# Optimization experiments

Hardware: AMD Instinct MI355X
Metric: run time of the kernel (lower is better)

## Reference

```python
import jax, jax.numpy as jnp
import numpy as np


def setup_inputs() -> dict:
    key = jax.random.key(0)
    kx, kw, kb = jax.random.split(key, 3)
    x = jax.random.normal(kx, (4, 2048, 4096), dtype=jnp.float32)
    weight = jax.random.normal(kw, (4096, 4096), dtype=jnp.float32) * 0.02
    bias = jax.random.normal(kb, (4096,), dtype=jnp.float32) * 0.02
    return {"x": x, "weight": weight, "bias": bias}


def _binarize_except_outliers(w):
    # Outlier mask from global weight stats (computed from w itself; in torch it
    # is cached after the first call but the values are identical every step).
    mean = jnp.mean(w)
    std = jnp.std(w, ddof=1)  # torch.std default is the unbiased estimator
    lower = mean - 1.96 * std
    upper = mean + 1.96 * std
    outliers = (w < lower) | (w > upper)
    keep = (~outliers).astype(w.dtype)
    # scaling_factor in the torch code: w[~outliers].abs().mean(-1) on the
    # flattened masked-select -> a single SCALAR, detached from the graph.
    scale = jax.lax.stop_gradient(jnp.sum(jnp.abs(w) * keep) / jnp.sum(keep))
    # NOTE: the torch code assigns STE-sign values and then immediately
    # overwrites them with w * scale, so the effective math is:
    w_bin = jnp.where(outliers, w, w * scale)
    return w_bin


def reference(x, weight, bias):
    w_bin = _binarize_except_outliers(weight)  # [out, in]
    # F.linear(x, w, b) = x @ w.T + b
    return jnp.einsum("bsi,oi->bso", x, w_bin) + bias
```

## Files before the change

### kernel.cpp

```cpp
#include <hip/hip_runtime.h>
#include <hip/hip_bf16.h>
#include <math.h>

#define MDIM 8192
#define NDIM 4096
#define KDIM 4096
#define WELEMS 16777216
#define XELEMS 33554432

typedef __attribute__((ext_vector_type(8))) short bf16x8;
typedef __attribute__((ext_vector_type(4))) float f32x4;

__device__ __forceinline__ unsigned short f2bf(float f) {
  unsigned int u = __float_as_uint(f);
  u += 0x7fffu + ((u >> 16) & 1u);
  return (unsigned short)(u >> 16);
}

__device__ __forceinline__ void gload16(const void* g, void* l) {
  __builtin_amdgcn_global_load_lds(
      (const __attribute__((address_space(1))) void*)g,
      (__attribute__((address_space(3))) void*)l, 16, 0, 0);
}

template <int MODE>
__global__ __launch_bounds__(256)
void np_stage1(const float* __restrict__ w, float* __restrict__ C,
               float* __restrict__ C2, const float* __restrict__ scal) {
  __shared__ float ls[32], ls2[32];
  const int t = threadIdx.x;
  const int leaf = t >> 3, j = t & 7;
  const size_t base = (size_t)blockIdx.x * 4096 + leaf * 128 + j;
  float mean = 0.f, lower = 0.f, upper = 0.f;
  if (MODE == 1) mean = scal[0];
  if (MODE == 2) { lower = scal[1]; upper = scal[2]; }
  float r = 0.f, r2 = 0.f;
#pragma unroll
  for (int s = 0; s < 16; s++) {
    float v = w[base + s * 8];
    float tv, tv2 = 0.f;
    if (MODE == 0) tv = v;
    else if (MODE == 1) { float x = v - mean; tv = __fmul_rn(x, x); }
    else {
      bool keep = !(v < lower || v > upper);
      tv = keep ? fabsf(v) : 0.f;
      tv2 = keep ? 1.f : 0.f;
    }
    if (s == 0) { r = tv; r2 = tv2; } else { r += tv; r2 += tv2; }
  }
  r += __shfl_xor(r, 1); r += __shfl_xor(r, 2); r += __shfl_xor(r, 4);
  if (MODE == 2) { r2 += __shfl_xor(r2, 1); r2 += __shfl_xor(r2, 2); r2 += __shfl_xor(r2, 4); }
  if (j == 0) { ls[leaf] = r; if (MODE == 2) ls2[leaf] = r2; }
  __syncthreads();
  if (t == 0) {
    float tmp[32];
    for (int i = 0; i < 32; i++) tmp[i] = ls[i];
    for (int n = 32; n > 1; n >>= 1)
      for (int i = 0; i < n / 2; i++) tmp[i] = tmp[2 * i] + tmp[2 * i + 1];
    C[blockIdx.x] = tmp[0];
    if (MODE == 2) {
      for (int i = 0; i < 32; i++) tmp[i] = ls2[i];
      for (int n = 32; n > 1; n >>= 1)
        for (int i = 0; i < n / 2; i++) tmp[i] = tmp[2 * i] + tmp[2 * i + 1];
      C2[blockIdx.x] = tmp[0];
    }
  }
}

template <int MODE>
__global__ __launch_bounds__(256)
void np_stage2(const float* __restrict__ C, const float* __restrict__ C2,
               float* __restrict__ scal) {
  __shared__ float ls[256], ls2[256];
  const int t = threadIdx.x;
  {
    float v[16];
    for (int i = 0; i < 16; i++) v[i] = C[t * 16 + i];
    for (int n = 16; n > 1; n >>= 1)
      for (int i = 0; i < n / 2; i++) v[i] = v[2 * i] + v[2 * i + 1];
    ls[t] = v[0];
    if (MODE == 2) {
      for (int i = 0; i < 16; i++) v[i] = C2[t * 16 + i];
      for (int n = 16; n > 1; n >>= 1)
        for (int i = 0; i < n / 2; i++) v[i] = v[2 * i] + v[2 * i + 1];
      ls2[t] = v[0];
    }
  }
  __syncthreads();
  if (t == 0) {
    float tmp[256];
    for (int i = 0; i < 256; i++) tmp[i] = ls[i];
    for (int n = 256; n > 1; n >>= 1)
      for (int i = 0; i < n / 2; i++) tmp[i] = tmp[2 * i] + tmp[2 * i + 1];
    float S = tmp[0];
    if (MODE == 0) {
      scal[0] = S / 16777216.0f;
    } else if (MODE == 1) {
      float var = S / 16777215.0f;
      float sd = sqrtf(var);
      float mean = scal[0];
      scal[1] = mean - __fmul_rn(1.96f, sd);
      scal[2] = mean + __fmul_rn(1.96f, sd);
    } else {
      for (int i = 0; i < 256; i++) tmp[i] = ls2[i];
      for (int n = 256; n > 1; n >>= 1)
        for (int i = 0; i < n / 2; i++) tmp[i] = tmp[2 * i] + tmp[2 * i + 1];
      scal[3] = S / tmp[0];
    }
  }
}

__device__ __forceinline__ void pack8(const float* __restrict__ p, unsigned short* dst,
                                      bool dobin, float lower, float upper, float scale) {
  float4 u = *(const float4*)p;
  float4 v = *(const float4*)(p + 4);
  float f[8] = {u.x, u.y, u.z, u.w, v.x, v.y, v.z, v.w};
  unsigned int r[4];
#pragma unroll
  for (int j = 0; j < 4; j++) {
    float a = f[2 * j], b = f[2 * j + 1];
    if (dobin) {
      bool oa = (a < lower) || (a > upper);
      bool ob = (b < lower) || (b > upper);
      a = oa ? a : __fmul_rn(a, scale);
      b = ob ? b : __fmul_rn(b, scale);
    }
    r[j] = (unsigned int)f2bf(a) | ((unsigned int)f2bf(b) << 16);
  }
  *(uint4*)dst = make_uint4(r[0], r[1], r[2], r[3]);
}

__global__ __launch_bounds__(256)
void convert_w(const float* __restrict__ w, unsigned short* __restrict__ wb,
               const float* __restrict__ scal) {
  float lower = scal[1], upper = scal[2], scale = scal[3];
  int tid = blockIdx.x * blockDim.x + threadIdx.x;
  int nth = gridDim.x * blockDim.x;
  int nc = WELEMS / 8;
  for (int i = tid; i < nc; i += nth)
    pack8(w + (size_t)i * 8, wb + (size_t)i * 8, true, lower, upper, scale);
}

__global__ __launch_bounds__(256)
void convert_x(const float* __restrict__ x, unsigned short* __restrict__ xb) {
  int tid = blockIdx.x * blockDim.x + threadIdx.x;
  int nth = gridDim.x * blockDim.x;
  int nc = XELEMS / 8;
  for (int i = tid; i < nc; i += nth)
    pack8(x + (size_t)i * 8, xb + (size_t)i * 8, false, 0.f, 0.f, 0.f);
}


#define VM6  asm volatile("s_waitcnt vmcnt(6)" ::: "memory")
#define VM0  asm volatile("s_waitcnt vmcnt(0)" ::: "memory")
#define LGK8 asm volatile("s_waitcnt lgkmcnt(8)" ::: "memory")
#define PSYNC { asm volatile("" ::: "memory"); __builtin_amdgcn_s_barrier(); asm volatile("" ::: "memory"); }

#define LDA(buf, mh) { \
  a[0][0] = *(const bf16x8*)&sA[buf][wm][((mh)*64 +  0 + fr)*64 + koo0]; \
  a[0][1] = *(const bf16x8*)&sA[buf][wm][((mh)*64 +  0 + fr)*64 + koo1]; \
  a[1][0] = *(const bf16x8*)&sA[buf][wm][((mh)*64 + 16 + fr)*64 + koo0]; \
  a[1][1] = *(const bf16x8*)&sA[buf][wm][((mh)*64 + 16 + fr)*64 + koo1]; \
  a[2][0] = *(const bf16x8*)&sA[buf][wm][((mh)*64 + 32 + fr)*64 + koo0]; \
  a[2][1] = *(const bf16x8*)&sA[buf][wm][((mh)*64 + 32 + fr)*64 + koo1]; \
  a[3][0] = *(const bf16x8*)&sA[buf][wm][((mh)*64 + 48 + fr)*64 + koo0]; \
  a[3][1] = *(const bf16x8*)&sA[buf][wm][((mh)*64 + 48 + fr)*64 + koo1]; }

#define LDBX(buf, nh, bb) { \
  bb[0][0] = *(const bf16x8*)&sB[buf][wnh][(wnq*64 + (nh)*32 +  0 + fr)*64 + koo0]; \
  bb[0][1] = *(const bf16x8*)&sB[buf][wnh][(wnq*64 + (nh)*32 +  0 + fr)*64 + koo1]; \
  bb[1][0] = *(const bf16x8*)&sB[buf][wnh][(wnq*64 + (nh)*32 + 16 + fr)*64 + koo0]; \
  bb[1][1] = *(const bf16x8*)&sB[buf][wnh][(wnq*64 + (nh)*32 + 16 + fr)*64 + koo1]; }

#define MM1(m, n, ks, bb) acc[m][n] = __builtin_amdgcn_mfma_f32_16x16x32_bf16(a[(m)&3][ks], bb[(n)&1][ks], acc[m][n], 0, 0, 0)
#define MMKS(mh, nh, ks, bb) { \
  MM1((mh)*4+0, (nh)*2+0, ks, bb); MM1((mh)*4+0, (nh)*2+1, ks, bb); \
  MM1((mh)*4+1, (nh)*2+0, ks, bb); MM1((mh)*4+1, (nh)*2+1, ks, bb); \
  MM1((mh)*4+2, (nh)*2+0, ks, bb); MM1((mh)*4+2, (nh)*2+1, ks, bb); \
  MM1((mh)*4+3, (nh)*2+0, ks, bb); MM1((mh)*4+3, (nh)*2+1, ks, bb); }
#define MM(mh, nh, bb) { \
  __builtin_amdgcn_s_setprio(1); \
  MMKS(mh, nh, 0, bb); MMKS(mh, nh, 1, bb); \
  __builtin_amdgcn_s_setprio(0); }

#define STGA(buf, q, ku) { \
  gload16(xbp + aoff[0][q] + (ku), &sA[buf][0][(q)*4096 + t8]); \
  gload16(xbp + aoff[1][q] + (ku), &sA[buf][1][(q)*4096 + t8]); }
#define STGB(buf, h, ku) { \
  gload16(wbp + boff[h][0] + (ku), &sB[buf][h][t8]); \
  gload16(wbp + boff[h][1] + (ku), &sB[buf][h][4096 + t8]); }

__global__ __launch_bounds__(512, 2)
void gemm256(const unsigned short* __restrict__ xbp, const unsigned short* __restrict__ wbp,
             const float* __restrict__ bias, float* __restrict__ out) {
  __shared__ unsigned short sA[2][2][8192];
  __shared__ unsigned short sB[2][2][8192];

  const int bid = blockIdx.x;
  const int swz = (bid & 7) * 64 + (bid >> 3);
  const int bm = swz >> 4;
  const int bn = swz & 15;

  const int t = threadIdx.x;
  const int lane = t & 63;
  const int wid = t >> 6;
  const int wm = wid >> 2;
  const int wn = wid & 3;
  const int wnh = wn >> 1;
  const int wnq = wn & 1;
  const int fr = lane & 15;
  const int ko = (lane >> 4) * 8;
  const int xr = (fr & 7) << 3;
  const int koo0 = ko ^ xr;
  const int koo1 = (32 + ko) ^ xr;

  const int t8 = t * 8;
  const int rl = t >> 3;
  const int cs = ((t & 7) * 8) ^ ((rl & 7) << 3);
  size_t aoff[2][2], boff[2][2];
#pragma unroll
  for (int h = 0; h < 2; h++)
#pragma unroll
    for (int q = 0; q < 2; q++) {
      aoff[h][q] = (size_t)(bm * 256 + h * 128 + q * 64 + rl) * KDIM + cs;
      boff[h][q] = (size_t)(bn * 256 + h * 128 + q * 64 + rl) * KDIM + cs;
    }

  f32x4 acc[8][4];
#pragma unroll
  for (int i = 0; i < 8; i++)
#pragma unroll
    for (int j = 0; j < 4; j++) acc[i][j] = {0.f, 0.f, 0.f, 0.f};

  bf16x8 a[4][2], b0[2][2], b1[2][2];

  STGB(0, 0, 0); STGB(0, 1, 0); STGA(0, 0, 0); STGA(0, 1, 0);
  STGB(1, 0, 64); STGB(1, 1, 64); STGA(1, 0, 64);
  VM6; PSYNC;

  const int NIT = KDIM / 128;
  for (int it = 0; it < NIT; ++it) {
    const bool last = (it == NIT - 1);
    const int kuB = it * 128 + 64;
    const int kuN = kuB + 64;
    const int kuL = kuB + 128;

    LDA(0, 0); LDBX(0, 0, b0);
    STGA(1, 1, kuB);
    LGK8; PSYNC;
    MM(0, 0, b0); PSYNC;

    LDBX(0, 1, b1);
    PSYNC;
    MM(0, 1, b1); PSYNC;

    LDA(0, 1);
    if (!last) { STGB(0, 0, kuN); STGB(0, 1, kuN); }
    PSYNC;
    MM(1, 1, b1); PSYNC;

    if (!last) STGA(0, 0, kuN);
    if (last) { VM0; } else { VM6; }
    PSYNC;
    MM(1, 0, b0); PSYNC;

    LDA(1, 0); LDBX(1, 0, b0);
    if (!last) STGA(0, 1, kuN);
    LGK8; PSYNC;
    MM(0, 0, b0); PSYNC;

    LDBX(1, 1, b1);
    PSYNC;
    MM(0, 1, b1); PSYNC;

    LDA(1, 1);
    if (!last) { STGB(1, 0, kuL); STGB(1, 1, kuL); }
    PSYNC;
    MM(1, 1, b1); PSYNC;

    if (!last) { STGA(1, 0, kuL); VM6; }
    PSYNC;
    MM(1, 0, b0); PSYNC;
  }

#pragma unroll
  for (int nn = 0; nn < 4; ++nn) {
    const int col = bn * 256 + wn * 64 + nn * 16 + (lane & 15);
    const float bv = bias[col];
#pragma unroll
    for (int m = 0; m < 8; ++m) {
      const int row0 = bm * 256 + wm * 128 + m * 16 + (lane >> 4) * 4;
#pragma unroll
      for (int q = 0; q < 4; ++q)
        out[(size_t)(row0 + q) * NDIM + col] = acc[m][nn][q] + bv;
    }
  }
}

template <bool A_BF16, bool B_BF16>
__global__ __launch_bounds__(256)
void gemm_bt(const void* __restrict__ Av, const void* __restrict__ Bv,
             const float* __restrict__ bias, float* __restrict__ out,
             const float* __restrict__ scal) {
  __shared__ unsigned short sAt[2][128 * 32];
  __shared__ unsigned short sBt[2][128 * 32];
  float lower = 0.f, upper = 0.f, scale = 0.f;
  if constexpr (!B_BF16) { lower = scal[1]; upper = scal[2]; scale = scal[3]; }
  const unsigned short* Ab = (const unsigned short*)Av;
  const float* Af = (const float*)Av;
  const unsigned short* Bb = (const unsigned short*)Bv;
  const float* Bf = (const float*)Bv;
  int bid = blockIdx.x;
  int swz = (bid & 7) * 256 + (bid >> 3);
  int bm = swz >> 5, bn = swz & 31;
  const int t = threadIdx.x, lane = t & 63, wid = t >> 6;
  const int wm = wid >> 1, wn = wid & 1;
  const int e0 = t * 8, e1 = e0 + 2048;
  const size_t aOff0 = (size_t)(bm * 128 + (e0 >> 5)) * KDIM + (e0 & 31);
  const size_t aOff1 = (size_t)(bm * 128 + (e1 >> 5)) * KDIM + (e1 & 31);
  const size_t bOff0 = (size_t)(bn * 128 + (e0 >> 5)) * KDIM + (e0 & 31);
  const size_t bOff1 = (size_t)(bn * 128 + (e1 >> 5)) * KDIM + (e1 & 31);
  f32x4 acc[4][4];
#pragma unroll
  for (int i = 0; i < 4; i++)
#pragma unroll
    for (int j = 0; j < 4; j++) acc[i][j] = {0.f, 0.f, 0.f, 0.f};
  auto stage = [&](int buf, int k0) {
    if constexpr (A_BF16) {
      gload16(Ab + aOff0 + k0, &sAt[buf][e0]);
      gload16(Ab + aOff1 + k0, &sAt[buf][e1]);
    } else {
      pack8(Af + aOff0 + k0, &sAt[buf][e0], false, 0.f, 0.f, 0.f);
      pack8(Af + aOff1 + k0, &sAt[buf][e1], false, 0.f, 0.f, 0.f);
    }
    if constexpr (B_BF16) {
      gload16(Bb + bOff0 + k0, &sBt[buf][e0]);
      gload16(Bb + bOff1 + k0, &sBt[buf][e1]);
    } else {
      pack8(Bf + bOff0 + k0, &sBt[buf][e0], true, lower, upper, scale);
      pack8(Bf + bOff1 + k0, &sBt[buf][e1], true, lower, upper, scale);
    }
  };
  stage(0, 0);
  const int NT = KDIM / 32;
  const int ko = (lane >> 4) * 8, fr = lane & 15;
  for (int tt = 0; tt < NT; ++tt) {
    int cur = tt & 1;
    __syncthreads();
    if (tt + 1 < NT) stage(cur ^ 1, (tt + 1) * 32);
    bf16x8 a[4], b[4];
#pragma unroll
    for (int i = 0; i < 4; i++) {
      a[i] = *(const bf16x8*)&sAt[cur][(wm * 64 + i * 16 + fr) * 32 + ko];
      b[i] = *(const bf16x8*)&sBt[cur][(wn * 64 + i * 16 + fr) * 32 + ko];
    }
#pragma unroll
    for (int i = 0; i < 4; i++)
#pragma unroll
      for (int j = 0; j < 4; j++)
        acc[i][j] = __builtin_amdgcn_mfma_f32_16x16x32_bf16(a[i], b[j], acc[i][j], 0, 0, 0);
  }
  const int colbase = bn * 128 + wn * 64 + (lane & 15);
  const int rowbase = bm * 128 + wm * 64 + (lane >> 4) * 4;
#pragma unroll
  for (int j = 0; j < 4; j++) {
    int col = colbase + j * 16;
    float bv = bias[col];
#pragma unroll
    for (int i = 0; i < 4; i++) {
      int row0 = rowbase + i * 16;
#pragma unroll
      for (int q = 0; q < 4; q++)
        out[(size_t)(row0 + q) * NDIM + col] = acc[i][j][q] + bv;
    }
  }
}

extern "C" void kernel_launch(void* const* d_in, const int* in_sizes, int n_in,
                              void* d_out, int out_size, void* d_ws, size_t ws_size,
                              hipStream_t stream) {
  const float* x = (const float*)d_in[0];
  const float* w = (const float*)d_in[1];
  const float* bias = (const float*)d_in[2];
  float* out = (float*)d_out;
  char* ws = (char*)d_ws;

  const size_t xb_b = (size_t)XELEMS * 2;
  const size_t wb_b = (size_t)WELEMS * 2;
  const size_t c_b = 4 * 4096 * sizeof(float);
  const bool full = ws_size >= xb_b + wb_b + c_b + 64;
  const bool wonly = !full && ws_size >= wb_b + c_b + 64;

  unsigned short *xb = nullptr, *wb = nullptr;
  float *C1, *scal;
  if (full) {
    xb = (unsigned short*)ws;
    wb = (unsigned short*)(ws + xb_b);
    C1 = (float*)(ws + xb_b + wb_b);
  } else if (wonly) {
    wb = (unsigned short*)ws;
    C1 = (float*)(ws + wb_b);
  } else {
    C1 = (float*)ws;
  }
  float* C2 = C1 + 4096;
  float* C3 = C2 + 4096;
  float* C4 = C3 + 4096;
  scal = C4 + 4096;

  np_stage1<0><<<dim3(4096), dim3(256), 0, stream>>>(w, C1, nullptr, scal);
  np_stage2<0><<<dim3(1), dim3(256), 0, stream>>>(C1, nullptr, scal);
  np_stage1<1><<<dim3(4096), dim3(256), 0, stream>>>(w, C2, nullptr, scal);
  np_stage2<1><<<dim3(1), dim3(256), 0, stream>>>(C2, nullptr, scal);
  np_stage1<2><<<dim3(4096), dim3(256), 0, stream>>>(w, C3, C4, scal);
  np_stage2<2><<<dim3(1), dim3(256), 0, stream>>>(C3, C4, scal);

  if (full) {
    convert_w<<<dim3(2048), dim3(256), 0, stream>>>(w, wb, scal);
    convert_x<<<dim3(4096), dim3(256), 0, stream>>>(x, xb);
    gemm256<<<dim3(512), dim3(512), 0, stream>>>(xb, wb, bias, out);
  } else if (wonly) {
    convert_w<<<dim3(2048), dim3(256), 0, stream>>>(w, wb, scal);
    gemm_bt<false, true><<<dim3(2048), dim3(256), 0, stream>>>(x, wb, bias, out, scal);
  } else {
    gemm_bt<false, false><<<dim3(2048), dim3(256), 0, stream>>>(x, w, bias, out, scal);
  }
}
```

Measured before the change: 414.3 us.

## Restructure GEMM main loop with double-buffered A fragments and one barrier per phase

Rewrites the bf16 MFMA main loop so each phase issues its LDS fragment reads for the next quarter-tile before the current MFMA block. Double A register sets (aE/aO) let the reads overlap compute, and one barrier per phase replaces the two used before. Global-to-LDS prefetch now uses 32-bit offsets that are advanced incrementally, and LDS addresses come from precomputed base pointers to cut address arithmetic. The cost is more VGPRs for the extra fragment set, which may cause spills at two blocks per CU, plus the risk of LDS read/write races because fewer barriers fence buffer reuse.

```diff
diff --git a/kernel.cpp b/kernel.cpp
--- a/kernel.cpp
+++ b/kernel.cpp
@@ -151,44 +151,44 @@
 }
 
 
-#define VM6  asm volatile("s_waitcnt vmcnt(6)" ::: "memory")
-#define VM0  asm volatile("s_waitcnt vmcnt(0)" ::: "memory")
-#define LGK8 asm volatile("s_waitcnt lgkmcnt(8)" ::: "memory")
+#define VM8  asm volatile("s_waitcnt vmcnt(8)" ::: "memory")
 #define PSYNC { asm volatile("" ::: "memory"); __builtin_amdgcn_s_barrier(); asm volatile("" ::: "memory"); }
 
-#define LDA(buf, mh) { \
-  a[0][0] = *(const bf16x8*)&sA[buf][wm][((mh)*64 +  0 + fr)*64 + koo0]; \
-  a[0][1] = *(const bf16x8*)&sA[buf][wm][((mh)*64 +  0 + fr)*64 + koo1]; \
-  a[1][0] = *(const bf16x8*)&sA[buf][wm][((mh)*64 + 16 + fr)*64 + koo0]; \
-  a[1][1] = *(const bf16x8*)&sA[buf][wm][((mh)*64 + 16 + fr)*64 + koo1]; \
-  a[2][0] = *(const bf16x8*)&sA[buf][wm][((mh)*64 + 32 + fr)*64 + koo0]; \
-  a[2][1] = *(const bf16x8*)&sA[buf][wm][((mh)*64 + 32 + fr)*64 + koo1]; \
-  a[3][0] = *(const bf16x8*)&sA[buf][wm][((mh)*64 + 48 + fr)*64 + koo0]; \
-  a[3][1] = *(const bf16x8*)&sA[buf][wm][((mh)*64 + 48 + fr)*64 + koo1]; }
-
-#define LDBX(buf, nh, bb) { \
-  bb[0][0] = *(const bf16x8*)&sB[buf][wnh][(wnq*64 + (nh)*32 +  0 + fr)*64 + koo0]; \
-  bb[0][1] = *(const bf16x8*)&sB[buf][wnh][(wnq*64 + (nh)*32 +  0 + fr)*64 + koo1]; \
-  bb[1][0] = *(const bf16x8*)&sB[buf][wnh][(wnq*64 + (nh)*32 + 16 + fr)*64 + koo0]; \
-  bb[1][1] = *(const bf16x8*)&sB[buf][wnh][(wnq*64 + (nh)*32 + 16 + fr)*64 + koo1]; }
-
-#define MM1(m, n, ks, bb) acc[m][n] = __builtin_amdgcn_mfma_f32_16x16x32_bf16(a[(m)&3][ks], bb[(n)&1][ks], acc[m][n], 0, 0, 0)
-#define MMKS(mh, nh, ks, bb) { \
-  MM1((mh)*4+0, (nh)*2+0, ks, bb); MM1((mh)*4+0, (nh)*2+1, ks, bb); \
-  MM1((mh)*4+1, (nh)*2+0, ks, bb); MM1((mh)*4+1, (nh)*2+1, ks, bb); \
-  MM1((mh)*4+2, (nh)*2+0, ks, bb); MM1((mh)*4+2, (nh)*2+1, ks, bb); \
-  MM1((mh)*4+3, (nh)*2+0, ks, bb); MM1((mh)*4+3, (nh)*2+1, ks, bb); }
-#define MM(mh, nh, bb) { \
+#define LDA(dst, buf, mh) do { \
+  dst[0][0] = *(const bf16x8*)(pA[buf][0] + ((mh)*64 +  0)*64); \
+  dst[0][1] = *(const bf16x8*)(pA[buf][1] + ((mh)*64 +  0)*64); \
+  dst[1][0] = *(const bf16x8*)(pA[buf][0] + ((mh)*64 + 16)*64); \
+  dst[1][1] = *(const bf16x8*)(pA[buf][1] + ((mh)*64 + 16)*64); \
+  dst[2][0] = *(const bf16x8*)(pA[buf][0] + ((mh)*64 + 32)*64); \
+  dst[2][1] = *(const bf16x8*)(pA[buf][1] + ((mh)*64 + 32)*64); \
+  dst[3][0] = *(const bf16x8*)(pA[buf][0] + ((mh)*64 + 48)*64); \
+  dst[3][1] = *(const bf16x8*)(pA[buf][1] + ((mh)*64 + 48)*64); } while (0)
+
+#define LDB(dst, buf, nh) do { \
+  dst[0][0] = *(const bf16x8*)(pB[buf][0] + ((nh)*32 +  0)*64); \
+  dst[0][1] = *(const bf16x8*)(pB[buf][1] + ((nh)*32 +  0)*64); \
+  dst[1][0] = *(const bf16x8*)(pB[buf][0] + ((nh)*32 + 16)*64); \
+  dst[1][1] = *(const bf16x8*)(pB[buf][1] + ((nh)*32 + 16)*64); } while (0)
+
+#define MM1(m, n, ks, A, B) acc[m][n] = __builtin_amdgcn_mfma_f32_16x16x32_bf16(A[(m)&3][ks], B[(n)&1][ks], acc[m][n], 0, 0, 0)
+#define MMQ(mh, nh, A, B) do { \
   __builtin_amdgcn_s_setprio(1); \
-  MMKS(mh, nh, 0, bb); MMKS(mh, nh, 1, bb); \
-  __builtin_amdgcn_s_setprio(0); }
-
-#define STGA(buf, q, ku) { \
-  gload16(xbp + aoff[0][q] + (ku), &sA[buf][0][(q)*4096 + t8]); \
-  gload16(xbp + aoff[1][q] + (ku), &sA[buf][1][(q)*4096 + t8]); }
-#define STGB(buf, h, ku) { \
-  gload16(wbp + boff[h][0] + (ku), &sB[buf][h][t8]); \
-  gload16(wbp + boff[h][1] + (ku), &sB[buf][h][4096 + t8]); }
+  MM1((mh)*4+0, (nh)*2+0, 0, A, B); MM1((mh)*4+0, (nh)*2+1, 0, A, B); \
+  MM1((mh)*4+1, (nh)*2+0, 0, A, B); MM1((mh)*4+1, (nh)*2+1, 0, A, B); \
+  MM1((mh)*4+2, (nh)*2+0, 0, A, B); MM1((mh)*4+2, (nh)*2+1, 0, A, B); \
+  MM1((mh)*4+3, (nh)*2+0, 0, A, B); MM1((mh)*4+3, (nh)*2+1, 0, A, B); \
+  MM1((mh)*4+0, (nh)*2+0, 1, A, B); MM1((mh)*4+0, (nh)*2+1, 1, A, B); \
+  MM1((mh)*4+1, (nh)*2+0, 1, A, B); MM1((mh)*4+1, (nh)*2+1, 1, A, B); \
+  MM1((mh)*4+2, (nh)*2+0, 1, A, B); MM1((mh)*4+2, (nh)*2+1, 1, A, B); \
+  MM1((mh)*4+3, (nh)*2+0, 1, A, B); MM1((mh)*4+3, (nh)*2+1, 1, A, B); \
+  __builtin_amdgcn_s_setprio(0); } while (0)
+
+#define STGA(buf, q, kadd) do { \
+  gload16(xbp + aofA[0][q] + (kadd), &sA[buf][0][(q)*4096 + t8]); \
+  gload16(xbp + aofA[1][q] + (kadd), &sA[buf][1][(q)*4096 + t8]); } while (0)
+#define STGB(buf, h, kadd) do { \
+  gload16(wbp + bofB[h][0] + (kadd), &sB[buf][h][t8]); \
+  gload16(wbp + bofB[h][1] + (kadd), &sB[buf][h][4096 + t8]); } while (0)
 
 __global__ __launch_bounds__(512, 2)
 void gemm256(const unsigned short* __restrict__ xbp, const unsigned short* __restrict__ wbp,
@@ -198,32 +198,39 @@
 
   const int bid = blockIdx.x;
   const int swz = (bid & 7) * 64 + (bid >> 3);
-  const int bm = swz >> 4;
-  const int bn = swz & 15;
+  const int bm = swz >> 4, bn = swz & 15;
 
   const int t = threadIdx.x;
   const int lane = t & 63;
   const int wid = t >> 6;
-  const int wm = wid >> 2;
-  const int wn = wid & 3;
-  const int wnh = wn >> 1;
-  const int wnq = wn & 1;
+  const int wm = wid >> 2, wn = wid & 3;
+  const int wnh = wn >> 1, wnq = wn & 1;
   const int fr = lane & 15;
   const int ko = (lane >> 4) * 8;
   const int xr = (fr & 7) << 3;
   const int koo0 = ko ^ xr;
   const int koo1 = (32 + ko) ^ xr;
 
+  const unsigned short* pA[2][2];
+  const unsigned short* pB[2][2];
+#pragma unroll
+  for (int buf = 0; buf < 2; ++buf) {
+    pA[buf][0] = &sA[buf][wm][fr * 64 + koo0];
+    pA[buf][1] = &sA[buf][wm][fr * 64 + koo1];
+    pB[buf][0] = &sB[buf][wnh][(wnq * 64 + fr) * 64 + koo0];
+    pB[buf][1] = &sB[buf][wnh][(wnq * 64 + fr) * 64 + koo1];
+  }
+
   const int t8 = t * 8;
   const int rl = t >> 3;
   const int cs = ((t & 7) * 8) ^ ((rl & 7) << 3);
-  size_t aoff[2][2], boff[2][2];
+  unsigned int aofA[2][2], bofB[2][2];
 #pragma unroll
   for (int h = 0; h < 2; h++)
 #pragma unroll
     for (int q = 0; q < 2; q++) {
-      aoff[h][q] = (size_t)(bm * 256 + h * 128 + q * 64 + rl) * KDIM + cs;
-      boff[h][q] = (size_t)(bn * 256 + h * 128 + q * 64 + rl) * KDIM + cs;
+      aofA[h][q] = (unsigned int)((bm * 256 + h * 128 + q * 64 + rl) * KDIM + cs);
+      bofB[h][q] = (unsigned int)((bn * 256 + h * 128 + q * 64 + rl) * KDIM + cs);
     }
 
   f32x4 acc[8][4];
@@ -232,55 +239,72 @@
 #pragma unroll
     for (int j = 0; j < 4; j++) acc[i][j] = {0.f, 0.f, 0.f, 0.f};
 
-  bf16x8 a[4][2], b0[2][2], b1[2][2];
-
-  STGB(0, 0, 0); STGB(0, 1, 0); STGA(0, 0, 0); STGA(0, 1, 0);
-  STGB(1, 0, 64); STGB(1, 1, 64); STGA(1, 0, 64);
-  VM6; PSYNC;
+  bf16x8 aE[4][2], aO[4][2], b0[2][2], b1[2][2];
+
+  STGA(0, 0, 0); STGB(0, 0, 0); STGB(0, 1, 0); STGA(0, 1, 0);
+  STGA(1, 0, 64); STGB(1, 0, 64); STGB(1, 1, 64); STGA(1, 1, 64);
+  VM8;
+  PSYNC;
+  LDA(aE, 0, 0); LDB(b0, 0, 0);
+#pragma unroll
+  for (int h = 0; h < 2; h++)
+#pragma unroll
+    for (int q = 0; q < 2; q++) { aofA[h][q] += 128; bofB[h][q] += 128; }
 
   const int NIT = KDIM / 128;
   for (int it = 0; it < NIT; ++it) {
-    const bool last = (it == NIT - 1);
-    const int kuB = it * 128 + 64;
-    const int kuN = kuB + 64;
-    const int kuL = kuB + 128;
-
-    LDA(0, 0); LDBX(0, 0, b0);
-    STGA(1, 1, kuB);
-    LGK8; PSYNC;
-    MM(0, 0, b0); PSYNC;
-
-    LDBX(0, 1, b1);
-    PSYNC;
-    MM(0, 1, b1); PSYNC;
-
-    LDA(0, 1);
-    if (!last) { STGB(0, 0, kuN); STGB(0, 1, kuN); }
-    PSYNC;
-    MM(1, 1, b1); PSYNC;
-
-    if (!last) STGA(0, 0, kuN);
-    if (last) { VM0; } else { VM6; }
-    PSYNC;
-    MM(1, 0, b0); PSYNC;
-
-    LDA(1, 0); LDBX(1, 0, b0);
-    if (!last) STGA(0, 1, kuN);
-    LGK8; PSYNC;
-    MM(0, 0, b0); PSYNC;
-
-    LDBX(1, 1, b1);
-    PSYNC;
-    MM(0, 1, b1); PSYNC;
-
-    LDA(1, 1);
-    if (!last) { STGB(1, 0, kuL); STGB(1, 1, kuL); }
-    PSYNC;
-    MM(1, 1, b1); PSYNC;
-
-    if (!last) { STGA(1, 0, kuL); VM6; }
-    PSYNC;
-    MM(1, 0, b0); PSYNC;
+    const bool nl = (it < NIT - 1);
+
+    PSYNC;
+    LDB(b1, 0, 1);
+    MMQ(0, 0, aE, b0);
+    VM8;
+
+    PSYNC;
+    LDA(aO, 0, 1);
+    if (nl) STGA(0, 0, 0);
+    MMQ(0, 1, aE, b1);
+    VM8;
+
+    PSYNC;
+    LDA(aE, 1, 0);
+    if (nl) { STGB(0, 0, 0); STGB(0, 1, 0); }
+    MMQ(1, 1, aO, b1);
+    VM8;
+
+    PSYNC;
+    LDB(b1, 1, 1);
+    if (nl) STGA(0, 1, 0);
+    MMQ(1, 0, aO, b0);
+
+    PSYNC;
+    LDB(b0, 1, 0);
+    MMQ(0, 1, aE, b1);
+    VM8;
+
+    PSYNC;
+    LDA(aO, 1, 1);
+    if (nl) STGA(1, 0, 64);
+    MMQ(0, 0, aE, b0);
+    VM8;
+
+    PSYNC;
+    if (nl) LDA(aE, 0, 0);
+    if (nl) { STGB(1, 0, 64); STGB(1, 1, 64); }
+    MMQ(1, 0, aO, b0);
+    VM8;
+
+    PSYNC;
+    if (nl) LDB(b0, 0, 0);
+    if (nl) STGA(1, 1, 64);
+    MMQ(1, 1, aO, b1);
+
+    if (nl) {
+#pragma unroll
+      for (int h = 0; h < 2; h++)
+#pragma unroll
+        for (int q = 0; q < 2; q++) { aofA[h][q] += 128; bofB[h][q] += 128; }
+    }
   }
 
 #pragma unroll
```

New measurement: 980.3 us. 2.37x slower.
